# Performance work log

Hardware: AMD Instinct MI355X
Metric: run time of the kernel (lower is better)

## Reference

```python
import jax, jax.numpy as jnp
import numpy as np

B, LQ, LK, H, DK, DV, E = 4, 1024, 1024, 12, 64, 768, 768
TOPK = 64
TEMP = 0.5
NEG = -10000.0


def setup_inputs() -> dict:
    key = jax.random.key(0)
    ks = jax.random.split(key, 10)
    s = 0.02  # weight init scale
    return {
        "q": jax.random.normal(ks[0], (B, LQ, E), jnp.float32),
        "k": jax.random.normal(ks[1], (B, LK, E), jnp.float32),
        "v": jax.random.normal(ks[2], (B, LK, DV), jnp.float32),
        "qpos": jnp.zeros((B, LQ), jnp.int32),
        "kpos": jnp.zeros((B, LK), jnp.int32),
        "qk_mask": jax.random.normal(ks[3], (B, 1, LQ, LK), jnp.float32) * 0.1,
        "k_mask": jax.random.normal(ks[4], (B, 1, LK, 1), jnp.float32) * 0.1,
        "post_softmax_mask": (jax.random.uniform(ks[5], (B, 1, LQ, LK)) > 0.1).astype(jnp.float32),
        "w_qs": jax.random.normal(ks[6], (E, H * DK), jnp.float32) * s,
        "w_ks": jax.random.normal(ks[7], (E, H * DK), jnp.float32) * s,
        "w_vs": jax.random.normal(ks[8], (DV, H * DV), jnp.float32) * s,
        "fc": jax.random.normal(ks[9], (H * DV, DV), jnp.float32) * s,
    }


def reference(q, k, v, qpos, kpos, qk_mask, k_mask, post_softmax_mask, w_qs, w_ks, w_vs, fc):
    residual = v
    # project and split heads: [b, len, h, d] -> [b, h, len, d]
    qh = (q @ w_qs).reshape(B, LQ, H, DK).transpose(0, 2, 1, 3)
    kh = (k @ w_ks).reshape(B, LK, H, DK).transpose(0, 2, 1, 3)
    vh = (v @ w_vs).reshape(B, LK, H, DV).transpose(0, 2, 1, 3)

    # scaled dot-product scores [b, h, lq, lk]
    attn = jnp.einsum('bhqd,bhkd->bhqk', qh / np.float32(np.sqrt(DK)), kh)
    attn = attn + qk_mask                              # additive qk mask
    attn = attn + jnp.squeeze(k_mask, -1)[:, :, None, :]  # additive key mask

    # topk sparsification: keep top-k scores, fill rest with -10000
    topk_vals, topk_idx = jax.lax.top_k(attn, TOPK)
    attn = jnp.put_along_axis(jnp.full_like(attn, NEG), topk_idx, topk_vals,
                              axis=-1, inplace=False)

    # temperature + stable softmax in fp32
    attn = attn / max(TEMP, 1e-6)
    attn = jax.nn.softmax(attn.astype(jnp.float32), axis=-1).astype(v.dtype)

    # post-softmax multiplicative mask + renorm (renorm_post_mask=True)
    attn = attn * post_softmax_mask
    attn = attn / jnp.maximum(attn.sum(axis=-1, keepdims=True), 1e-6)

    # straight-through argmax hardening (use_argmax=True)
    hard = jax.nn.one_hot(jnp.argmax(attn, axis=-1), LK, dtype=attn.dtype)
    attn = hard - jax.lax.stop_gradient(attn) + attn

    # attend, merge heads, output projection + residual (dropout=0)
    head_output = jnp.einsum('bhqk,bhkd->bhqd', attn, vh)
    output = head_output.transpose(0, 2, 1, 3).reshape(B, LQ, H * DV) @ fc
    output = output + residual
    return (output, attn)
```

## Files before the change

### kernel.cpp

```cpp
#include <hip/hip_runtime.h>

constexpr int NB  = 4;
constexpr int NH  = 12;
constexpr int SEQ = 1024;
constexpr int DKd = 64;
constexpr int DVd = 768;
constexpr int Ed  = 768;
constexpr int HVd = 9216;

typedef float f32x4 __attribute__((ext_vector_type(4)));
typedef short s16x8 __attribute__((ext_vector_type(8)));

__device__ __forceinline__ unsigned short f2bf(float f) {
  unsigned int u = __builtin_bit_cast(unsigned int, f);
  u += 0x7fffu + ((u >> 16) & 1u);
  return (unsigned short)(u >> 16);
}

__device__ __forceinline__ float bf2f_lo(unsigned int u) {
  return __builtin_bit_cast(float, u << 16);
}
__device__ __forceinline__ float bf2f_hi(unsigned int u) {
  return __builtin_bit_cast(float, u & 0xffff0000u);
}

__device__ __forceinline__ f32x4 mfma_bf16_16x16x32(s16x8 a, s16x8 b, f32x4 c) {
  asm("v_mfma_f32_16x16x32_bf16 %0, %1, %2, %0" : "+v"(c) : "v"(a), "v"(b));
  return c;
}

#define GLOAD16(g, l)                                                          \
  __builtin_amdgcn_global_load_lds(                                            \
      (const __attribute__((address_space(1))) unsigned int*)(g),              \
      (__attribute__((address_space(3))) unsigned int*)(l), 16, 0, 0)

__global__ __launch_bounds__(256)
void cvt_bf16_kernel(const float* __restrict__ v, unsigned short* __restrict__ Vbf, int n4) {
  int i = blockIdx.x * 256 + threadIdx.x;
  const int stride = gridDim.x * 256;
  for (; i < n4; i += stride) {
    const f32x4 x = *(const f32x4*)&v[(size_t)i * 4];
    uint2 u;
    u.x = (unsigned)f2bf(x[0]) | ((unsigned)f2bf(x[1]) << 16);
    u.y = (unsigned)f2bf(x[2]) | ((unsigned)f2bf(x[3]) << 16);
    *(uint2*)&Vbf[(size_t)i * 4] = u;
  }
}

__global__ __launch_bounds__(256)
void qkproj_kernel(const float* __restrict__ q, const float* __restrict__ k,
                   const float* __restrict__ w_qs, const float* __restrict__ w_ks,
                   float* __restrict__ qh, float* __restrict__ kh) {
  const float* A  = blockIdx.z ? k : q;
  const float* Bw = blockIdx.z ? w_ks : w_qs;
  float* C        = blockIdx.z ? kh : qh;
  __shared__ float As[16][68];
  __shared__ float Bs[16][68];
  const int tid = threadIdx.x;
  const int m0 = blockIdx.x * 64, n0 = blockIdx.y * 64;
  const int ty = tid >> 4, tx = tid & 15;
  const int arow = tid >> 2, akc = (tid & 3) * 4;
  const int bkr = tid >> 4, bnc = (tid & 15) * 4;

  float acc[4][4];
#pragma unroll
  for (int i = 0; i < 4; i++)
#pragma unroll
    for (int j = 0; j < 4; j++) acc[i][j] = 0.f;

  for (int k0 = 0; k0 < 768; k0 += 16) {
    const f32x4 av = *(const f32x4*)&A[(size_t)(m0 + arow) * 768 + k0 + akc];
    const f32x4 bv = *(const f32x4*)&Bw[(size_t)(k0 + bkr) * 768 + n0 + bnc];
    __syncthreads();
#pragma unroll
    for (int c = 0; c < 4; c++) As[akc + c][arow] = av[c];
    *(f32x4*)&Bs[bkr][bnc] = bv;
    __syncthreads();
#pragma unroll
    for (int kk = 0; kk < 16; kk++) {
      const f32x4 a = *(const f32x4*)&As[kk][ty * 4];
      const f32x4 b = *(const f32x4*)&Bs[kk][tx * 4];
#pragma unroll
      for (int i = 0; i < 4; i++)
#pragma unroll
        for (int j = 0; j < 4; j++) acc[i][j] += a[i] * b[j];
    }
  }
#pragma unroll
  for (int i = 0; i < 4; i++) {
    f32x4 o;
#pragma unroll
    for (int j = 0; j < 4; j++) o[j] = acc[i][j];
    *(f32x4*)&C[(size_t)(m0 + ty * 4 + i) * 768 + n0 + tx * 4] = o;
  }
}

__global__ __launch_bounds__(256)
void score_argmax_kernel(const float* __restrict__ qh, const float* __restrict__ kh,
                         const float* __restrict__ qk_mask, const float* __restrict__ k_mask,
                         const float* __restrict__ pmask, float2* __restrict__ partials) {
  __shared__ float QsT[64][128];
  __shared__ float KsT[64][128];
  const int bh = blockIdx.z;
  const int b = bh / NH, h = bh % NH;
  const int q0 = blockIdx.y * 128;
  const int k0 = blockIdx.x * 128;
  const int tid = threadIdx.x;
  const int ty = tid >> 4, tx = tid & 15;

  const int row = tid >> 1;
  const int cb = (tid & 1) * 32;
  const float* qsrc = qh + (size_t)(b * SEQ + q0 + row) * Ed + h * DKd + cb;
  const float* ksrc = kh + (size_t)(b * SEQ + k0 + row) * Ed + h * DKd + cb;
#pragma unroll
  for (int i = 0; i < 8; i++) {
    const f32x4 qv = *(const f32x4*)&qsrc[4 * i];
    const f32x4 kv = *(const f32x4*)&ksrc[4 * i];
#pragma unroll
    for (int c = 0; c < 4; c++) {
      QsT[cb + 4 * i + c][row] = qv[c];
      KsT[cb + 4 * i + c][row] = kv[c];
    }
  }
  __syncthreads();

  float acc[8][8];
#pragma unroll
  for (int i = 0; i < 8; i++)
#pragma unroll
    for (int j = 0; j < 8; j++) acc[i][j] = 0.f;

#pragma unroll 8
  for (int kk = 0; kk < 64; kk++) {
    const f32x4 a0 = *(const f32x4*)&QsT[kk][ty * 8];
    const f32x4 a1 = *(const f32x4*)&QsT[kk][ty * 8 + 4];
    const f32x4 b0 = *(const f32x4*)&KsT[kk][tx * 8];
    const f32x4 b1 = *(const f32x4*)&KsT[kk][tx * 8 + 4];
#pragma unroll
    for (int i = 0; i < 4; i++)
#pragma unroll
      for (int j = 0; j < 4; j++) {
        acc[i][j]         += a0[i] * b0[j];
        acc[i][j + 4]     += a0[i] * b1[j];
        acc[i + 4][j]     += a1[i] * b0[j];
        acc[i + 4][j + 4] += a1[i] * b1[j];
      }
  }

  const int kg0 = k0 + tx * 8;
  const f32x4 km0 = *(const f32x4*)&k_mask[b * SEQ + kg0];
  const f32x4 km1 = *(const f32x4*)&k_mask[b * SEQ + kg0 + 4];
#pragma unroll
  for (int i = 0; i < 8; i++) {
    const int qg = q0 + ty * 8 + i;
    const size_t base = (size_t)(b * SEQ + qg) * SEQ + kg0;
    const f32x4 qm0 = *(const f32x4*)&qk_mask[base];
    const f32x4 qm1 = *(const f32x4*)&qk_mask[base + 4];
    const f32x4 pm0 = *(const f32x4*)&pmask[base];
    const f32x4 pm1 = *(const f32x4*)&pmask[base + 4];
    float bv = -3.0e38f;
    int bi = 0;
#pragma unroll
    for (int j = 0; j < 4; j++) {
      const float s = acc[i][j] * 0.125f + qm0[j] + km0[j];
      if (pm0[j] > 0.f && s > bv) { bv = s; bi = kg0 + j; }
    }
#pragma unroll
    for (int j = 0; j < 4; j++) {
      const float s = acc[i][4 + j] * 0.125f + qm1[j] + km1[j];
      if (pm1[j] > 0.f && s > bv) { bv = s; bi = kg0 + 4 + j; }
    }
#pragma unroll
    for (int off = 1; off < 16; off <<= 1) {
      const float ov = __shfl_xor(bv, off);
      const int   oi = __shfl_xor(bi, off);
      if (ov > bv || (ov == bv && oi < bi)) { bv = ov; bi = oi; }
    }
    if (tx == 0)
      partials[(size_t)(bh * SEQ + qg) * 8 + blockIdx.x] =
          make_float2(bv, __int_as_float(bi));
  }
}

__global__ __launch_bounds__(256)
void argmax_reduce_kernel(const float2* __restrict__ partials, int* __restrict__ kmaxp) {
  const int t = blockIdx.x * 256 + threadIdx.x;
  if (t >= NB * NH * SEQ) return;
  const float2* p = partials + (size_t)t * 8;
  float bv = -3.0e38f;
  int bi = 0;
#pragma unroll
  for (int i = 0; i < 8; i++) {
    const float vv = p[i].x;
    const int ii = __float_as_int(p[i].y);
    if (vv > bv) { bv = vv; bi = ii; }
  }
  kmaxp[t] = bi;
}

__global__ __launch_bounds__(256)
void wvfc_gemm_kernel(const float* __restrict__ wvs, const float* __restrict__ fcw,
                      unsigned short* __restrict__ MstbT) {
  __shared__ unsigned short As[128][72];
  __shared__ unsigned short Bs[128][72];
  const int tid = threadIdx.x;
  const int h = blockIdx.z;
  const int m0 = blockIdx.x * 128, n0 = blockIdx.y * 128;
  const int wid = tid >> 6, lane = tid & 63;
  const int wr = (wid >> 1) * 64, wc = (wid & 1) * 64;
  const int lm = lane & 15, lq = lane >> 4;
  const int ar = tid >> 1, acb = (tid & 1) * 32;
  const int br = tid >> 2, bnb = (tid & 3) * 32;

  f32x4 acc[4][4];
#pragma unroll
  for (int m = 0; m < 4; m++)
#pragma unroll
    for (int n = 0; n < 4; n++)
#pragma unroll
      for (int r = 0; r < 4; r++) acc[m][n][r] = 0.f;

  for (int k0 = 0; k0 < 768; k0 += 64) {
    const float* asrc = wvs + (size_t)(m0 + ar) * HVd + h * 768 + k0 + acb;
    const float* bsrc = fcw + (size_t)(h * 768 + k0 + br) * 768 + n0 + bnb;
    f32x4 a4[8], b4[8];
#pragma unroll
    for (int i = 0; i < 8; i++) a4[i] = *(const f32x4*)&asrc[4 * i];
#pragma unroll
    for (int i = 0; i < 8; i++) b4[i] = *(const f32x4*)&bsrc[4 * i];
    __syncthreads();
#pragma unroll
    for (int i = 0; i < 4; i++) {
      s16x8 pk;
#pragma unroll
      for (int j = 0; j < 8; j++) pk[j] = (short)f2bf(a4[2 * i + (j >> 2)][j & 3]);
      *(s16x8*)&As[ar][acb + 8 * i] = pk;
    }
#pragma unroll
    for (int i = 0; i < 8; i++)
#pragma unroll
      for (int c = 0; c < 4; c++) Bs[bnb + 4 * i + c][br] = f2bf(b4[i][c]);
    __syncthreads();
#pragma unroll
    for (int ks = 0; ks < 2; ks++) {
      s16x8 af[4], bfr[4];
#pragma unroll
      for (int m = 0; m < 4; m++)
        af[m] = *(const s16x8*)&As[wr + m * 16 + lm][ks * 32 + lq * 8];
#pragma unroll
      for (int n = 0; n < 4; n++)
        bfr[n] = *(const s16x8*)&Bs[wc + n * 16 + lm][ks * 32 + lq * 8];
#pragma unroll
      for (int m = 0; m < 4; m++)
#pragma unroll
        for (int n = 0; n < 4; n++)
          acc[m][n] = mfma_bf16_16x16x32(af[m], bfr[n], acc[m][n]);
    }
  }
  asm volatile("s_nop 7\n\ts_nop 7");
#pragma unroll
  for (int m = 0; m < 4; m++)
#pragma unroll
    for (int n = 0; n < 4; n++) {
      const int grow0 = m0 + wr + m * 16 + lq * 4;
      const int gcol  = n0 + wc + n * 16 + lm;
      uint2 u;
      u.x = (unsigned)f2bf(acc[m][n][0]) | ((unsigned)f2bf(acc[m][n][1]) << 16);
      u.y = (unsigned)f2bf(acc[m][n][2]) | ((unsigned)f2bf(acc[m][n][3]) << 16);
      *(uint2*)&MstbT[(size_t)(h * 768 + gcol) * 768 + grow0] = u;
    }
}

__global__ __launch_bounds__(256)
void ugemm_kernel(const unsigned short* __restrict__ Vbf,
                  const unsigned short* __restrict__ MstbT,
                  unsigned short* __restrict__ U, int h0) {
  __shared__ unsigned short As[128 * 64];
  __shared__ unsigned short Bs[128 * 64];
  const int tid = threadIdx.x;
  const int h = h0 + blockIdx.z;
  const int m0 = blockIdx.x * 128, n0 = blockIdx.y * 128;
  const int wid = tid >> 6, lane = tid & 63;
  const int wr = (wid >> 1) * 64, wc = (wid & 1) * 64;
  const int lm = lane & 15, lq = lane >> 4;
  const int srow = tid >> 3, scol = (tid & 7) * 8;
  const int ldst = (tid >> 6) * 512;

  const unsigned short* asrc = Vbf + (size_t)(m0 + srow) * 768 + scol;
  const unsigned short* bsrc = MstbT + (size_t)(h * 768 + n0 + srow) * 768 + scol;

  f32x4 acc[4][4];
#pragma unroll
  for (int m = 0; m < 4; m++)
#pragma unroll
    for (int n = 0; n < 4; n++)
#pragma unroll
      for (int r = 0; r < 4; r++) acc[m][n][r] = 0.f;

  for (int k0 = 0; k0 < 768; k0 += 64) {
#pragma unroll
    for (int j = 0; j < 4; j++)
      GLOAD16(asrc + (size_t)j * 32 * 768 + k0, &As[j * 2048 + ldst]);
#pragma unroll
    for (int j = 0; j < 4; j++)
      GLOAD16(bsrc + (size_t)j * 32 * 768 + k0, &Bs[j * 2048 + ldst]);
    __syncthreads();
#pragma unroll
    for (int ks = 0; ks < 2; ks++) {
      s16x8 af[4], bfr[4];
#pragma unroll
      for (int m = 0; m < 4; m++)
        af[m] = *(const s16x8*)&As[(wr + m * 16 + lm) * 64 + ks * 32 + lq * 8];
#pragma unroll
      for (int n = 0; n < 4; n++)
        bfr[n] = *(const s16x8*)&Bs[(wc + n * 16 + lm) * 64 + ks * 32 + lq * 8];
#pragma unroll
      for (int m = 0; m < 4; m++)
#pragma unroll
        for (int n = 0; n < 4; n++)
          acc[m][n] = mfma_bf16_16x16x32(af[m], bfr[n], acc[m][n]);
    }
    __syncthreads();
  }
  asm volatile("s_nop 7\n\ts_nop 7");
  const size_t urow0 = (size_t)blockIdx.z * 4096;
#pragma unroll
  for (int m = 0; m < 4; m++)
#pragma unroll
    for (int r = 0; r < 4; r++) {
      const int row = m0 + wr + m * 16 + lq * 4 + r;
      uint2 u;
      u.x = (unsigned)f2bf(acc[m][0][r]) | ((unsigned)f2bf(acc[m][1][r]) << 16);
      u.y = (unsigned)f2bf(acc[m][2][r]) | ((unsigned)f2bf(acc[m][3][r]) << 16);
      *(uint2*)&U[(urow0 + row) * 768 + n0 + wc + lm * 4] = u;
    }
}

__global__ __launch_bounds__(192)
void gathersum_kernel(const unsigned short* __restrict__ U, const int* __restrict__ kmaxp,
                      const float* __restrict__ v, float* __restrict__ out0, int h0) {
  const int row = blockIdx.x;
  const int b = row >> 10, q = row & 1023;
  const int t = threadIdx.x;
  float a0 = 0.f, a1 = 0.f, a2 = 0.f, a3 = 0.f;
#pragma unroll
  for (int hg = 0; hg < 6; hg++) {
    const int g = kmaxp[((b * NH + h0 + hg) << 10) + q];
    const uint2 u = *(const uint2*)&U[((size_t)hg * 4096 + (b << 10) + g) * 768 + t * 4];
    a0 += bf2f_lo(u.x);
    a1 += bf2f_hi(u.x);
    a2 += bf2f_lo(u.y);
    a3 += bf2f_hi(u.y);
  }
  const int chunk = t >> 4, lmm = t & 15;
  const size_t ob = (size_t)row * 768 + chunk * 64 + lmm;
  if (h0 == 0) {
    out0[ob +  0] = a0 + v[ob +  0];
    out0[ob + 16] = a1 + v[ob + 16];
    out0[ob + 32] = a2 + v[ob + 32];
    out0[ob + 48] = a3 + v[ob + 48];
  } else {
    out0[ob +  0] += a0;
    out0[ob + 16] += a1;
    out0[ob + 32] += a2;
    out0[ob + 48] += a3;
  }
}

__global__ void zero_kernel(f32x4* __restrict__ p, int n4) {
  int i = blockIdx.x * blockDim.x + threadIdx.x;
  const int stride = gridDim.x * blockDim.x;
  f32x4 z;
  z[0] = z[1] = z[2] = z[3] = 0.f;
  for (; i < n4; i += stride) p[i] = z;
}

__global__ __launch_bounds__(256)
void scatter_kernel(const int* __restrict__ kmaxp, float* __restrict__ attn) {
  const int t = blockIdx.x * 256 + threadIdx.x;
  if (t >= NB * NH * SEQ) return;
  attn[((size_t)t << 10) + kmaxp[t]] = 1.0f;
}

extern "C" void kernel_launch(void* const* d_in, const int* in_sizes, int n_in,
                              void* d_out, int out_size, void* d_ws, size_t ws_size,
                              hipStream_t stream) {
  (void)in_sizes; (void)n_in; (void)out_size; (void)ws_size;
  const float* q       = (const float*)d_in[0];
  const float* k       = (const float*)d_in[1];
  const float* v       = (const float*)d_in[2];
  const float* qk_mask = (const float*)d_in[5];
  const float* k_mask  = (const float*)d_in[6];
  const float* pmask   = (const float*)d_in[7];
  const float* w_qs    = (const float*)d_in[8];
  const float* w_ks    = (const float*)d_in[9];
  const float* w_vs    = (const float*)d_in[10];
  const float* fc      = (const float*)d_in[11];

  float* out0 = (float*)d_out;
  float* attn = out0 + (size_t)NB * SEQ * DVd;

  char* ws = (char*)d_ws;
  unsigned short* MstbT = (unsigned short*)ws;
  unsigned short* Vbf   = (unsigned short*)(ws + 14155776);
  int* kmaxp            = (int*)(ws + 20447232);
  char* ureg            = ws + 20643840;
  unsigned short* U     = (unsigned short*)ureg;
  float* qh             = (float*)ureg;
  float* kh             = (float*)(ureg + 12582912);
  float2* partials      = (float2*)(ureg + 25165824);

  cvt_bf16_kernel<<<dim3(3072), 256, 0, stream>>>(v, Vbf, NB * SEQ * DVd / 4);

  qkproj_kernel<<<dim3(64, 12, 2), 256, 0, stream>>>(q, k, w_qs, w_ks, qh, kh);

  score_argmax_kernel<<<dim3(8, 8, NB * NH), 256, 0, stream>>>(
      qh, kh, qk_mask, k_mask, pmask, partials);
  argmax_reduce_kernel<<<dim3((NB * NH * SEQ + 255) / 256), 256, 0, stream>>>(partials, kmaxp);

  wvfc_gemm_kernel<<<dim3(6, 6, NH), 256, 0, stream>>>(w_vs, fc, MstbT);

  ugemm_kernel<<<dim3(32, 6, 6), 256, 0, stream>>>(Vbf, MstbT, U, 0);
  gathersum_kernel<<<dim3(NB * SEQ), 192, 0, stream>>>(U, kmaxp, v, out0, 0);
  ugemm_kernel<<<dim3(32, 6, 6), 256, 0, stream>>>(Vbf, MstbT, U, 6);
  gathersum_kernel<<<dim3(NB * SEQ), 192, 0, stream>>>(U, kmaxp, v, out0, 6);

  zero_kernel<<<dim3(2048), 256, 0, stream>>>((f32x4*)attn,
                                              (int)((size_t)NB * NH * SEQ * SEQ / 4));
  scatter_kernel<<<dim3((NB * NH * SEQ + 255) / 256), 256, 0, stream>>>(kmaxp, attn);
}
```

Before: 471.2 us.

## Premerge masks once, enlarge QK projection tiles, swizzle GEMM block order

Adds a pre-pass that folds qk_mask, k_mask and the post-softmax mask into one float buffer, so the per-head score kernel reads one mask array instead of three. The 12 heads previously re-read all three masks per batch. The QK projection moves from 64x64 to 128x128 tiles with 8x8 register blocking, for more reuse per load. The projection and U-GEMM kernels also get a block-index swizzle for L2 locality. The extra pass writes a 16MB buffer into workspace shared with MstbT and reorders launches, and raises register pressure in the projection kernel.

```diff
diff --git a/kernel.cpp b/kernel.cpp
--- a/kernel.cpp
+++ b/kernel.cpp
@@ -48,57 +48,88 @@
 }
 
 __global__ __launch_bounds__(256)
+void maskprep_kernel(const float* __restrict__ qk, const float* __restrict__ km,
+                     const float* __restrict__ pm, float* __restrict__ ms) {
+  const int i = blockIdx.x * 256 + threadIdx.x;
+  const int kk4 = i & 255;
+  const int b = i >> 18;
+  const f32x4 qv = *(const f32x4*)&qk[(size_t)i * 4];
+  const f32x4 pv = *(const f32x4*)&pm[(size_t)i * 4];
+  const f32x4 kv = *(const f32x4*)&km[b * SEQ + kk4 * 4];
+  f32x4 o;
+#pragma unroll
+  for (int c = 0; c < 4; c++) o[c] = pv[c] > 0.f ? qv[c] + kv[c] : -3.0e38f;
+  *(f32x4*)&ms[(size_t)i * 4] = o;
+}
+
+__global__ __launch_bounds__(256)
 void qkproj_kernel(const float* __restrict__ q, const float* __restrict__ k,
                    const float* __restrict__ w_qs, const float* __restrict__ w_ks,
                    float* __restrict__ qh, float* __restrict__ kh) {
   const float* A  = blockIdx.z ? k : q;
   const float* Bw = blockIdx.z ? w_ks : w_qs;
   float* C        = blockIdx.z ? kh : qh;
-  __shared__ float As[16][68];
-  __shared__ float Bs[16][68];
+  __shared__ float As[16][128];
+  __shared__ float Bs[16][128];
   const int tid = threadIdx.x;
-  const int m0 = blockIdx.x * 64, n0 = blockIdx.y * 64;
+  const int bx = (int)blockIdx.x;
+  const int sx = ((bx & 7) << 2) | (bx >> 3);
+  const int m0 = sx * 128, n0 = blockIdx.y * 128;
   const int ty = tid >> 4, tx = tid & 15;
-  const int arow = tid >> 2, akc = (tid & 3) * 4;
-  const int bkr = tid >> 4, bnc = (tid & 15) * 4;
-
-  float acc[4][4];
-#pragma unroll
-  for (int i = 0; i < 4; i++)
-#pragma unroll
-    for (int j = 0; j < 4; j++) acc[i][j] = 0.f;
+  const int arow = tid >> 1, akc = (tid & 1) * 8;
+  const int bkr = tid >> 4, bnc = (tid & 15) * 8;
+
+  float acc[8][8];
+#pragma unroll
+  for (int i = 0; i < 8; i++)
+#pragma unroll
+    for (int j = 0; j < 8; j++) acc[i][j] = 0.f;
 
   for (int k0 = 0; k0 < 768; k0 += 16) {
-    const f32x4 av = *(const f32x4*)&A[(size_t)(m0 + arow) * 768 + k0 + akc];
-    const f32x4 bv = *(const f32x4*)&Bw[(size_t)(k0 + bkr) * 768 + n0 + bnc];
-    __syncthreads();
-#pragma unroll
-    for (int c = 0; c < 4; c++) As[akc + c][arow] = av[c];
-    *(f32x4*)&Bs[bkr][bnc] = bv;
+    const f32x4 av0 = *(const f32x4*)&A[(size_t)(m0 + arow) * 768 + k0 + akc];
+    const f32x4 av1 = *(const f32x4*)&A[(size_t)(m0 + arow) * 768 + k0 + akc + 4];
+    const f32x4 bv0 = *(const f32x4*)&Bw[(size_t)(k0 + bkr) * 768 + n0 + bnc];
+    const f32x4 bv1 = *(const f32x4*)&Bw[(size_t)(k0 + bkr) * 768 + n0 + bnc + 4];
+    __syncthreads();
+#pragma unroll
+    for (int c = 0; c < 4; c++) {
+      As[akc + c][arow]     = av0[c];
+      As[akc + 4 + c][arow] = av1[c];
+    }
+    *(f32x4*)&Bs[bkr][bnc]     = bv0;
+    *(f32x4*)&Bs[bkr][bnc + 4] = bv1;
     __syncthreads();
 #pragma unroll
     for (int kk = 0; kk < 16; kk++) {
-      const f32x4 a = *(const f32x4*)&As[kk][ty * 4];
-      const f32x4 b = *(const f32x4*)&Bs[kk][tx * 4];
+      const f32x4 a0 = *(const f32x4*)&As[kk][ty * 8];
+      const f32x4 a1 = *(const f32x4*)&As[kk][ty * 8 + 4];
+      const f32x4 b0 = *(const f32x4*)&Bs[kk][tx * 8];
+      const f32x4 b1 = *(const f32x4*)&Bs[kk][tx * 8 + 4];
 #pragma unroll
       for (int i = 0; i < 4; i++)
 #pragma unroll
-        for (int j = 0; j < 4; j++) acc[i][j] += a[i] * b[j];
-    }
-  }
-#pragma unroll
-  for (int i = 0; i < 4; i++) {
-    f32x4 o;
-#pragma unroll
-    for (int j = 0; j < 4; j++) o[j] = acc[i][j];
-    *(f32x4*)&C[(size_t)(m0 + ty * 4 + i) * 768 + n0 + tx * 4] = o;
+        for (int j = 0; j < 4; j++) {
+          acc[i][j]         += a0[i] * b0[j];
+          acc[i][j + 4]     += a0[i] * b1[j];
+          acc[i + 4][j]     += a1[i] * b0[j];
+          acc[i + 4][j + 4] += a1[i] * b1[j];
+        }
+    }
+  }
+#pragma unroll
+  for (int i = 0; i < 8; i++) {
+    f32x4 o0, o1;
+#pragma unroll
+    for (int c = 0; c < 4; c++) { o0[c] = acc[i][c]; o1[c] = acc[i][4 + c]; }
+    const size_t rb = (size_t)(m0 + ty * 8 + i) * 768 + n0 + tx * 8;
+    *(f32x4*)&C[rb] = o0;
+    *(f32x4*)&C[rb + 4] = o1;
   }
 }
 
 __global__ __launch_bounds__(256)
 void score_argmax_kernel(const float* __restrict__ qh, const float* __restrict__ kh,
-                         const float* __restrict__ qk_mask, const float* __restrict__ k_mask,
-                         const float* __restrict__ pmask, float2* __restrict__ partials) {
+                         const float* __restrict__ ms, float2* __restrict__ partials) {
   __shared__ float QsT[64][128];
   __shared__ float KsT[64][128];
   const int bh = blockIdx.z;
@@ -148,27 +179,23 @@
   }
 
   const int kg0 = k0 + tx * 8;
-  const f32x4 km0 = *(const f32x4*)&k_mask[b * SEQ + kg0];
-  const f32x4 km1 = *(const f32x4*)&k_mask[b * SEQ + kg0 + 4];
 #pragma unroll
   for (int i = 0; i < 8; i++) {
     const int qg = q0 + ty * 8 + i;
     const size_t base = (size_t)(b * SEQ + qg) * SEQ + kg0;
-    const f32x4 qm0 = *(const f32x4*)&qk_mask[base];
-    const f32x4 qm1 = *(const f32x4*)&qk_mask[base + 4];
-    const f32x4 pm0 = *(const f32x4*)&pmask[base];
-    const f32x4 pm1 = *(const f32x4*)&pmask[base + 4];
+    const f32x4 ms0 = *(const f32x4*)&ms[base];
+    const f32x4 ms1 = *(const f32x4*)&ms[base + 4];
     float bv = -3.0e38f;
     int bi = 0;
 #pragma unroll
     for (int j = 0; j < 4; j++) {
-      const float s = acc[i][j] * 0.125f + qm0[j] + km0[j];
-      if (pm0[j] > 0.f && s > bv) { bv = s; bi = kg0 + j; }
+      const float s = acc[i][j] * 0.125f + ms0[j];
+      if (s > bv) { bv = s; bi = kg0 + j; }
     }
 #pragma unroll
     for (int j = 0; j < 4; j++) {
-      const float s = acc[i][4 + j] * 0.125f + qm1[j] + km1[j];
-      if (pm1[j] > 0.f && s > bv) { bv = s; bi = kg0 + 4 + j; }
+      const float s = acc[i][4 + j] * 0.125f + ms1[j];
+      if (s > bv) { bv = s; bi = kg0 + 4 + j; }
     }
 #pragma unroll
     for (int off = 1; off < 16; off <<= 1) {
@@ -279,7 +306,9 @@
   __shared__ unsigned short Bs[128 * 64];
   const int tid = threadIdx.x;
   const int h = h0 + blockIdx.z;
-  const int m0 = blockIdx.x * 128, n0 = blockIdx.y * 128;
+  const int bx = (int)blockIdx.x;
+  const int sx = ((bx & 7) << 2) | (bx >> 3);
+  const int m0 = sx * 128, n0 = blockIdx.y * 128;
   const int wid = tid >> 6, lane = tid & 63;
   const int wr = (wid >> 1) * 64, wc = (wid & 1) * 64;
   const int lm = lane & 15, lq = lane >> 4;
@@ -403,6 +432,7 @@
   char* ws = (char*)d_ws;
   unsigned short* MstbT = (unsigned short*)ws;
   unsigned short* Vbf   = (unsigned short*)(ws + 14155776);
+  float* msbuf          = (float*)ws;
   int* kmaxp            = (int*)(ws + 20447232);
   char* ureg            = ws + 20643840;
   unsigned short* U     = (unsigned short*)ureg;
@@ -410,13 +440,14 @@
   float* kh             = (float*)(ureg + 12582912);
   float2* partials      = (float2*)(ureg + 25165824);
 
+  maskprep_kernel<<<dim3(4096), 256, 0, stream>>>(qk_mask, k_mask, pmask, msbuf);
+
+  qkproj_kernel<<<dim3(32, 6, 2), 256, 0, stream>>>(q, k, w_qs, w_ks, qh, kh);
+
+  score_argmax_kernel<<<dim3(8, 8, NB * NH), 256, 0, stream>>>(qh, kh, msbuf, partials);
+  argmax_reduce_kernel<<<dim3((NB * NH * SEQ + 255) / 256), 256, 0, stream>>>(partials, kmaxp);
+
   cvt_bf16_kernel<<<dim3(3072), 256, 0, stream>>>(v, Vbf, NB * SEQ * DVd / 4);
-
-  qkproj_kernel<<<dim3(64, 12, 2), 256, 0, stream>>>(q, k, w_qs, w_ks, qh, kh);
-
-  score_argmax_kernel<<<dim3(8, 8, NB * NH), 256, 0, stream>>>(
-      qh, kh, qk_mask, k_mask, pmask, partials);
-  argmax_reduce_kernel<<<dim3((NB * NH * SEQ + 255) / 256), 256, 0, stream>>>(partials, kmaxp);
 
   wvfc_gemm_kernel<<<dim3(6, 6, NH), 256, 0, stream>>>(w_vs, fc, MstbT);
 
```

Measured after the change: 473.9 us. About the same (+0.6%).
